# Kernel optimization log

Hardware: AMD Instinct MI355X
Metric: run time of the kernel (lower is better)

## Reference

```python
import jax, jax.numpy as jnp
import numpy as np

B, CH_IN, D, H, W = 8, 256, 64, 16, 16
S = CH_IN // 2  # shurink = 128


def setup_inputs() -> dict:
    key = jax.random.key(0)
    ks = jax.random.split(key, 9)
    kstd = (2.0 / CH_IN) ** 0.5   # kaiming-like for 1x1 conv, fan_in = CH_IN
    ostd = (2.0 / S) ** 0.5
    x = jax.random.normal(ks[0], (B, CH_IN, D, H, W), dtype=jnp.float32)
    wk = jax.random.normal(ks[1], (S, CH_IN), dtype=jnp.float32) * kstd
    wq = jax.random.normal(ks[2], (S, CH_IN), dtype=jnp.float32) * kstd
    wv = jax.random.normal(ks[3], (S, CH_IN), dtype=jnp.float32) * kstd
    wo = jax.random.normal(ks[4], (CH_IN, S), dtype=jnp.float32) * ostd
    bk = jax.random.normal(ks[5], (S,), dtype=jnp.float32) * 0.01
    bq = jax.random.normal(ks[6], (S,), dtype=jnp.float32) * 0.01
    bv = jax.random.normal(ks[7], (S,), dtype=jnp.float32) * 0.01
    bo = jax.random.normal(ks[8], (CH_IN,), dtype=jnp.float32) * 0.01
    return {"x": x, "wk": wk, "bk": bk, "wq": wq, "bq": bq,
            "wv": wv, "bv": bv, "wo": wo, "bo": bo}


def reference(x, wk, bk, wq, bq, wv, bv, wo, bo):
    # 1x1x1 Conv3d == channel contraction: [B,C,D,H,W] x [S,C] -> [B,S,D,H,W]
    def proj(w, b):
        return jnp.einsum('bcdhw,oc->bodhw', x, w) + b[None, :, None, None, None]

    k = proj(wk, bk)  # [B,S,D,H,W]
    q = proj(wq, bq)
    v = proj(wv, bv)
    s_dim = k.shape[1]
    scale = 1.0 / jnp.sqrt(jnp.asarray(s_dim, x.dtype))
    # torch: bmm(k^T, q) over per-(b,h,w) [S,D] matrices -> [D_i, D_j]
    scores = jnp.einsum('bsihw,bsjhw->bhwij', k, q) * scale  # [B,H,W,D,D]
    # torch softmax(dim=1) on [BHW, D, D] == softmax over i (keys axis)
    a = jax.nn.softmax(scores, axis=3)
    # torch: bmm(v, a) -> [S, D_j]
    att = jnp.einsum('bsihw,bhwij->bsjhw', v, a)  # [B,S,D,H,W]
    out = jnp.einsum('bsdhw,cs->bcdhw', att, wo) + bo[None, :, None, None, None]
    return x + out  # atten_factor = 1
```

## Files before the change

### kernel.cpp

```cpp
#include <hip/hip_runtime.h>
#include <hip/hip_bf16.h>


typedef __bf16 bf16_t;
typedef bf16_t bf16x8 __attribute__((ext_vector_type(8)));
typedef bf16_t bf16x4 __attribute__((ext_vector_type(4)));
typedef float  f32x4  __attribute__((ext_vector_type(4)));

#define NB   8
#define NC   256
#define ND   64
#define NHW  256
#define NS   128

#define MFMA16 __builtin_amdgcn_mfma_f32_16x16x32_bf16

__device__ __forceinline__ int swz(int row, int col) {
  return col ^ ((row & 7) << 3);
}

__device__ __forceinline__ bf16x8 pack8(float4 a, float4 b) {
  bf16x8 r;
  r[0] = (bf16_t)a.x; r[1] = (bf16_t)a.y; r[2] = (bf16_t)a.z; r[3] = (bf16_t)a.w;
  r[4] = (bf16_t)b.x; r[5] = (bf16_t)b.y; r[6] = (bf16_t)b.z; r[7] = (bf16_t)b.w;
  return r;
}

__device__ __forceinline__ bf16x8 ldg_w8(const float* p) {
  float4 a = *(const float4*)p;
  float4 b = *(const float4*)(p + 4);
  return pack8(a, b);
}

__global__ __launch_bounds__(256) void transpose_x_w(
    const float* __restrict__ x,
    const float* __restrict__ wk, const float* __restrict__ wq,
    const float* __restrict__ wv, const float* __restrict__ wo,
    bf16_t* __restrict__ xT, bf16_t* __restrict__ wsW) {
  __shared__ bf16_t tile[64 * 72];
  const int bid = blockIdx.x;
  if (bid >= 8192) {
    const int wid = bid - 8192;
    const int mat = wid >> 3, sub = wid & 7;
    const int t = threadIdx.x;
    if (mat < 3) {
      const float* src = (mat == 0) ? wk : (mat == 1) ? wq : wv;
      bf16_t* dst = wsW + mat * 32768;
      int s = sub * 16 + (t >> 4), c0 = (t & 15) * 16;
      const float* p = src + s * NC + c0;
      float4 a0 = *(const float4*)p, a1 = *(const float4*)(p + 4);
      float4 a2 = *(const float4*)(p + 8), a3 = *(const float4*)(p + 12);
      *(bf16x8*)(dst + (c0 >> 3) * 1024 + s * 8)       = pack8(a0, a1);
      *(bf16x8*)(dst + ((c0 >> 3) + 1) * 1024 + s * 8) = pack8(a2, a3);
    } else {
      bf16_t* dst = wsW + 98304;
      int c = sub * 32 + (t >> 3), sc0 = (t & 7) * 16;
      const float* p = wo + c * NS + sc0;
      float4 a0 = *(const float4*)p, a1 = *(const float4*)(p + 4);
      float4 a2 = *(const float4*)(p + 8), a3 = *(const float4*)(p + 12);
      *(bf16x8*)(dst + (sc0 >> 3) * 2048 + c * 8)       = pack8(a0, a1);
      *(bf16x8*)(dst + ((sc0 >> 3) + 1) * 2048 + c * 8) = pack8(a2, a3);
    }
    return;
  }
  const int ct = bid & 3, hwt = (bid >> 2) & 3;
  const int d = (bid >> 4) & 63, b = bid >> 10;
  const int c0 = ct * 64, hw0 = hwt * 64;
  const int t = threadIdx.x;
  const int hwq = t & 15, chi = t >> 4;

  #pragma unroll
  for (int q = 0; q < 4; ++q) {
    int c = q * 16 + chi;
    float4 v4 = *(const float4*)(x + ((size_t)((b * NC + c0 + c) * ND + d)) * NHW + hw0 + hwq * 4);
    tile[(hwq * 4 + 0) * 72 + c] = (bf16_t)v4.x;
    tile[(hwq * 4 + 1) * 72 + c] = (bf16_t)v4.y;
    tile[(hwq * 4 + 2) * 72 + c] = (bf16_t)v4.z;
    tile[(hwq * 4 + 3) * 72 + c] = (bf16_t)v4.w;
  }
  __syncthreads();
  #pragma unroll
  for (int i = 0; i < 2; ++i) {
    int idx = t + 256 * i;
    int hw = idx >> 3, q = idx & 7;
    bf16x8 v8 = *(const bf16x8*)&tile[hw * 72 + q * 8];
    *(bf16x8*)(xT + ((size_t)((b * ND + d) * NHW + hw0 + hw)) * NC + c0 + q * 8) = v8;
  }
}

__global__ __launch_bounds__(256, 2) void qkv_attn2(
    const bf16_t* __restrict__ xT, const bf16_t* __restrict__ wsW,
    const float* __restrict__ bk, const float* __restrict__ bq,
    const float* __restrict__ bv, bf16_t* __restrict__ att) {
  __shared__ struct {
    union {
      bf16_t xTl[ND * NC];
      struct {
        bf16_t aT[ND * ND];
        bf16_t attT[ND * NS];
      } p2;
    } u;
    bf16_t kT[ND * NS];
    bf16_t qT[ND * NS];
    bf16_t vS[NS * ND];
  } sm;
  const int gid = blockIdx.x;
  const int b = gid & 7, hw = gid >> 3;
  const int t = threadIdx.x, w = t >> 6, lane = t & 63;
  const int l16 = lane & 15, q4 = lane >> 4;

  const bf16_t* wkF = wsW;
  const bf16_t* wqF = wsW + 32768;
  const bf16_t* wvF = wsW + 65536;

  #pragma unroll
  for (int jj = 0; jj < 8; ++jj) {
    int id = jj * 256 + t;
    int d = id >> 5, cg = (id & 31) * 8;
    bf16x8 v8 = *(const bf16x8*)(xT + ((size_t)((b * ND + d) * NHW + hw)) * NC + cg);
    *(bf16x8*)&sm.u.xTl[d * NC + swz(d, cg)] = v8;
  }
  __syncthreads();

  {
    const int mat = w >> 1;
    const int sb = (w & 1) * 64;
    const bf16_t* wm = mat ? wqF : wkF;
    const float* bm = mat ? bq : bk;
    bf16_t* dst = mat ? sm.qT : sm.kT;
    f32x4 acc[4][4] = {};
    for (int ks = 0; ks < 8; ++ks) {
      const int kb = ks * 32 + q4 * 8;
      bf16x8 afr[4];
      #pragma unroll
      for (int mt = 0; mt < 4; ++mt) {
        int s = sb + mt * 16 + l16;
        afr[mt] = *(const bf16x8*)(wm + (kb >> 3) * 1024 + s * 8);
      }
      #pragma unroll
      for (int nt = 0; nt < 4; ++nt) {
        int row = nt * 16 + l16;
        bf16x8 bfr = *(const bf16x8*)&sm.u.xTl[row * NC + swz(row, kb)];
        #pragma unroll
        for (int mt = 0; mt < 4; ++mt)
          acc[mt][nt] = MFMA16(afr[mt], bfr, acc[mt][nt], 0, 0, 0);
      }
    }
    #pragma unroll
    for (int mt = 0; mt < 4; ++mt) {
      int s0 = sb + mt * 16 + q4 * 4;
      float4 b4 = *(const float4*)(bm + s0);
      #pragma unroll
      for (int nt = 0; nt < 4; ++nt) {
        int d = nt * 16 + l16;
        bf16x4 pk;
        pk[0] = (bf16_t)(acc[mt][nt][0] + b4.x);
        pk[1] = (bf16_t)(acc[mt][nt][1] + b4.y);
        pk[2] = (bf16_t)(acc[mt][nt][2] + b4.z);
        pk[3] = (bf16_t)(acc[mt][nt][3] + b4.w);
        *(bf16x4*)&dst[d * NS + swz(d, s0)] = pk;
      }
    }
  }

  {
    const int sb = w * 32;
    f32x4 acc[4][2] = {};
    for (int ks = 0; ks < 8; ++ks) {
      const int kb = ks * 32 + q4 * 8;
      bf16x8 afr[4], bfr[2];
      #pragma unroll
      for (int mt = 0; mt < 4; ++mt) {
        int row = mt * 16 + l16;
        afr[mt] = *(const bf16x8*)&sm.u.xTl[row * NC + swz(row, kb)];
      }
      #pragma unroll
      for (int nt = 0; nt < 2; ++nt) {
        int s = sb + nt * 16 + l16;
        bfr[nt] = *(const bf16x8*)(wvF + (kb >> 3) * 1024 + s * 8);
      }
      #pragma unroll
      for (int nt = 0; nt < 2; ++nt)
        #pragma unroll
        for (int mt = 0; mt < 4; ++mt)
          acc[mt][nt] = MFMA16(afr[mt], bfr[nt], acc[mt][nt], 0, 0, 0);
    }
    #pragma unroll
    for (int nt = 0; nt < 2; ++nt) {
      int s = sb + nt * 16 + l16;
      float bvs = bv[s];
      #pragma unroll
      for (int mt = 0; mt < 4; ++mt) {
        int d0 = mt * 16 + q4 * 4;
        bf16x4 pv;
        pv[0] = (bf16_t)(acc[mt][nt][0] + bvs);
        pv[1] = (bf16_t)(acc[mt][nt][1] + bvs);
        pv[2] = (bf16_t)(acc[mt][nt][2] + bvs);
        pv[3] = (bf16_t)(acc[mt][nt][3] + bvs);
        *(bf16x4*)&sm.vS[s * ND + (d0 ^ ((s & 7) << 3))] = pv;
      }
    }
  }
  __syncthreads();

  {
    f32x4 sacc[4] = {};
    for (int ks = 0; ks < 4; ++ks) {
      const int kb = ks * 32 + q4 * 8;
      int jrow = w * 16 + l16;
      bf16x8 bfr = *(const bf16x8*)&sm.qT[jrow * NS + swz(jrow, kb)];
      #pragma unroll
      for (int it = 0; it < 4; ++it) {
        int irow = it * 16 + l16;
        bf16x8 afr = *(const bf16x8*)&sm.kT[irow * NS + swz(irow, kb)];
        sacc[it] = MFMA16(afr, bfr, sacc[it], 0, 0, 0);
      }
    }
    const float scale = 0.088388347648318447f;
    float ps[16];
    float mx = -1e30f;
    #pragma unroll
    for (int it = 0; it < 4; ++it)
      #pragma unroll
      for (int r = 0; r < 4; ++r) {
        float vv = sacc[it][r] * scale;
        ps[it * 4 + r] = vv;
        mx = fmaxf(mx, vv);
      }
    mx = fmaxf(mx, __shfl_xor(mx, 16));
    mx = fmaxf(mx, __shfl_xor(mx, 32));
    float sum = 0.f;
    #pragma unroll
    for (int i = 0; i < 16; ++i) { ps[i] = __expf(ps[i] - mx); sum += ps[i]; }
    sum += __shfl_xor(sum, 16);
    sum += __shfl_xor(sum, 32);
    float inv = 1.f / sum;
    int j = w * 16 + l16;
    #pragma unroll
    for (int it = 0; it < 4; ++it) {
      bf16x4 pk;
      #pragma unroll
      for (int r = 0; r < 4; ++r) pk[r] = (bf16_t)(ps[it * 4 + r] * inv);
      *(bf16x4*)&sm.u.p2.aT[j * ND + ((it * 16 + q4 * 4) ^ ((j & 7) << 3))] = pk;
    }
  }
  __syncthreads();

  {
    const int sb = w * 32;
    f32x4 acc[2][4] = {};
    #pragma unroll
    for (int ki = 0; ki < 2; ++ki) {
      const int kb = ki * 32 + q4 * 8;
      bf16x8 afr[2];
      #pragma unroll
      for (int mt = 0; mt < 2; ++mt) {
        int srow = sb + mt * 16 + l16;
        afr[mt] = *(const bf16x8*)&sm.vS[srow * ND + (kb ^ ((srow & 7) << 3))];
      }
      #pragma unroll
      for (int nt = 0; nt < 4; ++nt) {
        int jrow = nt * 16 + l16;
        bf16x8 bfr = *(const bf16x8*)&sm.u.p2.aT[jrow * ND + (kb ^ ((jrow & 7) << 3))];
        #pragma unroll
        for (int mt = 0; mt < 2; ++mt)
          acc[mt][nt] = MFMA16(afr[mt], bfr, acc[mt][nt], 0, 0, 0);
      }
    }
    #pragma unroll
    for (int nt = 0; nt < 4; ++nt) {
      int j = nt * 16 + l16;
      #pragma unroll
      for (int mt = 0; mt < 2; ++mt) {
        bf16x4 pk;
        #pragma unroll
        for (int r = 0; r < 4; ++r) pk[r] = (bf16_t)acc[mt][nt][r];
        *(bf16x4*)&sm.u.p2.attT[j * NS + swz(j, sb + mt * 16 + q4 * 4)] = pk;
      }
    }
  }
  __syncthreads();

  #pragma unroll
  for (int jj = 0; jj < 4; ++jj) {
    int f = jj * 2048 + t * 8;
    int d = f >> 7, s0 = f & 127;
    bf16x8 v8 = *(const bf16x8*)&sm.u.p2.attT[d * NS + (s0 ^ ((d & 7) << 3))];
    *(bf16x8*)(att + ((size_t)((b * ND + d) * NHW + hw)) * NS + s0) = v8;
  }
}

__global__ __launch_bounds__(256, 2) void out_proj(
    const bf16_t* __restrict__ att_ws,
    const bf16_t* __restrict__ woF, const float* __restrict__ bo,
    const float* __restrict__ x, float* __restrict__ out) {
  __shared__ union {
    bf16_t slab[256 * 128];
    float  stage[64 * 256];
  } sm;
  const int bid = blockIdx.x;
  const int ht = bid & 7, dc = (bid >> 3) & 7, ch = (bid >> 6) & 1, b = bid >> 7;
  const int t = threadIdx.x, w = t >> 6, lane = t & 63;
  const int l16 = lane & 15, g = lane >> 4;
  const int mh = w >> 1, nh = w & 1;

  {
    const int d = t >> 5, hw = t & 31;
    const bf16_t* src = att_ws + ((size_t)((b * ND + dc * 8 + d) * NHW + ht * 32 + hw)) * NS;
    const int row = d * 32 + hw;
    #pragma unroll
    for (int j = 0; j < 16; ++j) {
      bf16x8 v8 = *(const bf16x8*)(src + j * 8);
      *(bf16x8*)&sm.slab[row * NS + ((j ^ (hw & 7)) << 3)] = v8;
    }
  }
  __syncthreads();

  f32x4 acc[4][8] = {};
  #pragma unroll
  for (int kq = 0; kq < 4; ++kq) {
    bf16x8 af[4];
    #pragma unroll
    for (int mt = 0; mt < 4; ++mt) {
      int c = ch * 128 + mh * 64 + mt * 16 + l16;
      af[mt] = *(const bf16x8*)(woF + (kq * 4 + g) * 2048 + c * 8);
    }
    #pragma unroll
    for (int nt = 0; nt < 8; ++nt) {
      int dl = nh * 4 + (nt >> 1);
      int hwl = (nt & 1) * 16 + l16;
      int row = dl * 32 + hwl;
      bf16x8 bfr = *(const bf16x8*)&sm.slab[row * NS + (((kq * 4 + g) ^ (hwl & 7)) << 3)];
      #pragma unroll
      for (int mt = 0; mt < 4; ++mt)
        acc[mt][nt] = MFMA16(af[mt], bfr, acc[mt][nt], 0, 0, 0);
    }
  }

  #pragma unroll
  for (int p = 0; p < 2; ++p) {
    __syncthreads();
    if (mh == p) {
      #pragma unroll
      for (int mt = 0; mt < 4; ++mt) {
        #pragma unroll
        for (int nt = 0; nt < 8; ++nt) {
          int dl = nh * 4 + (nt >> 1);
          int hws = ((nt & 1) * 16 + l16) ^ (g << 3);
          int base = (mt * 16 + g * 4) * 256 + dl * 32 + hws;
          #pragma unroll
          for (int r = 0; r < 4; ++r)
            sm.stage[base + r * 256] = acc[mt][nt][r];
        }
      }
    }
    __syncthreads();
    #pragma unroll
    for (int ii = 0; ii < 16; ++ii) {
      int c6 = ii * 4 + w;
      int c = ch * 128 + p * 64 + c6;
      int dq = (lane >> 3) & 7;
      int hw4 = (lane & 7) * 4;
      float4 v = *(const float4*)&sm.stage[c6 * 256 + dq * 32 + (hw4 ^ ((ii & 3) << 3))];
      size_t gi = ((size_t)(b * NC + c) * ND + dc * 8 + dq) * NHW + ht * 32 + hw4;
      float4 xv = *(const float4*)(x + gi);
      float bias = bo[c];
      float4 o;
      o.x = v.x + bias + xv.x;
      o.y = v.y + bias + xv.y;
      o.z = v.z + bias + xv.z;
      o.w = v.w + bias + xv.w;
      *(float4*)(out + gi) = o;
    }
  }
}

struct SMemF {
  union {
    bf16_t xT[ND * NC];
    struct { bf16_t aT[ND * ND]; bf16_t attT[ND * NS]; } p2;
  } u;
  bf16_t kT[ND * NS];
  bf16_t qT[ND * NS];
  bf16_t vS[NS * ND];
};

__global__ __launch_bounds__(256) void attn_fused(
    const float* __restrict__ x,
    const float* __restrict__ wk, const float* __restrict__ bk,
    const float* __restrict__ wq, const float* __restrict__ bq,
    const float* __restrict__ wv, const float* __restrict__ bv,
    const float* __restrict__ wo, const float* __restrict__ bo,
    float* __restrict__ out) {
  __shared__ SMemF sm;
  const int gid = blockIdx.x;
  const int b = gid & 7;
  const int hw = gid >> 3;
  const int t = threadIdx.x;
  const int w = t >> 6;
  const int lane = t & 63;
  const int l16 = lane & 15;
  const int q4 = lane >> 4;
  const float* xb = x + (size_t)b * NC * ND * NHW + hw;
  {
    const int d = t & 63;
    const int cb = (t >> 6) * 64;
    for (int jj = 0; jj < 8; ++jj) {
      bf16x8 pk;
      #pragma unroll
      for (int e = 0; e < 8; ++e) {
        int c = cb + jj * 8 + e;
        pk[e] = (bf16_t)xb[(size_t)(c * ND + d) * NHW];
      }
      *(bf16x8*)&sm.u.xT[d * NC + swz(d, cb + jj * 8)] = pk;
    }
  }
  __syncthreads();
  {
    const int mat = w >> 1;
    const int sb = (w & 1) * 64;
    const float* wm = mat ? wq : wk;
    const float* bm = mat ? bq : bk;
    bf16_t* dst = mat ? sm.qT : sm.kT;
    f32x4 acc[4][4] = {};
    for (int ks = 0; ks < 8; ++ks) {
      const int kb = ks * 32 + q4 * 8;
      bf16x8 afr[4];
      #pragma unroll
      for (int mt = 0; mt < 4; ++mt) {
        int row = mt * 16 + l16;
        afr[mt] = *(const bf16x8*)&sm.u.xT[row * NC + swz(row, kb)];
      }
      #pragma unroll
      for (int st = 0; st < 4; ++st) {
        int s = sb + st * 16 + l16;
        bf16x8 bfr = ldg_w8(wm + s * NC + kb);
        #pragma unroll
        for (int mt = 0; mt < 4; ++mt)
          acc[mt][st] = MFMA16(afr[mt], bfr, acc[mt][st], 0, 0, 0);
      }
    }
    #pragma unroll
    for (int st = 0; st < 4; ++st) {
      int s = sb + st * 16 + l16;
      float bias = bm[s];
      #pragma unroll
      for (int mt = 0; mt < 4; ++mt) {
        #pragma unroll
        for (int r = 0; r < 4; ++r) {
          int d = mt * 16 + q4 * 4 + r;
          dst[d * NS + swz(d, s)] = (bf16_t)(acc[mt][st][r] + bias);
        }
      }
    }
  }
  {
    const int sb = w * 32;
    f32x4 acc[2][4] = {};
    for (int ks = 0; ks < 8; ++ks) {
      const int kb = ks * 32 + q4 * 8;
      bf16x8 afr[2];
      #pragma unroll
      for (int mt = 0; mt < 2; ++mt)
        afr[mt] = ldg_w8(wv + (sb + mt * 16 + l16) * NC + kb);
      #pragma unroll
      for (int nt = 0; nt < 4; ++nt) {
        int row = nt * 16 + l16;
        bf16x8 bfr = *(const bf16x8*)&sm.u.xT[row * NC + swz(row, kb)];
        #pragma unroll
        for (int mt = 0; mt < 2; ++mt)
          acc[mt][nt] = MFMA16(afr[mt], bfr, acc[mt][nt], 0, 0, 0);
      }
    }
    #pragma unroll
    for (int mt = 0; mt < 2; ++mt) {
      #pragma unroll
      for (int r = 0; r < 4; ++r) {
        int s = sb + mt * 16 + q4 * 4 + r;
        float bias = bv[s];
        #pragma unroll
        for (int nt = 0; nt < 4; ++nt) {
          int d = nt * 16 + l16;
          sm.vS[s * ND + swz(s, d)] = (bf16_t)(acc[mt][nt][r] + bias);
        }
      }
    }
  }
  __syncthreads();
  {
    f32x4 sacc[4] = {};
    for (int ks = 0; ks < 4; ++ks) {
      const int kb = ks * 32 + q4 * 8;
      int jrow = w * 16 + l16;
      bf16x8 bfr = *(const bf16x8*)&sm.qT[jrow * NS + swz(jrow, kb)];
      #pragma unroll
      for (int it = 0; it < 4; ++it) {
        int irow = it * 16 + l16;
        bf16x8 afr = *(const bf16x8*)&sm.kT[irow * NS + swz(irow, kb)];
        sacc[it] = MFMA16(afr, bfr, sacc[it], 0, 0, 0);
      }
    }
    const float scale = 0.088388347648318447f;
    float ps[16];
    float mx = -1e30f;
    #pragma unroll
    for (int it = 0; it < 4; ++it) {
      #pragma unroll
      for (int r = 0; r < 4; ++r) {
        float vv = sacc[it][r] * scale;
        ps[it * 4 + r] = vv;
        mx = fmaxf(mx, vv);
      }
    }
    mx = fmaxf(mx, __shfl_xor(mx, 16));
    mx = fmaxf(mx, __shfl_xor(mx, 32));
    float sum = 0.f;
    #pragma unroll
    for (int i = 0; i < 16; ++i) { ps[i] = __expf(ps[i] - mx); sum += ps[i]; }
    sum += __shfl_xor(sum, 16);
    sum += __shfl_xor(sum, 32);
    float inv = 1.f / sum;
    int j = w * 16 + l16;
    #pragma unroll
    for (int it = 0; it < 4; ++it) {
      bf16x4 pk;
      #pragma unroll
      for (int r = 0; r < 4; ++r) pk[r] = (bf16_t)(ps[it * 4 + r] * inv);
      *(bf16x4*)&sm.u.p2.aT[j * ND + swz(j, it * 16 + q4 * 4)] = pk;
    }
  }
  __syncthreads();
  {
    const int sb = w * 32;
    f32x4 acc[2][4] = {};
    #pragma unroll
    for (int ki = 0; ki < 2; ++ki) {
      const int kb = ki * 32 + q4 * 8;
      bf16x8 afr[2];
      #pragma unroll
      for (int mt = 0; mt < 2; ++mt) {
        int srow = sb + mt * 16 + l16;
        afr[mt] = *(const bf16x8*)&sm.vS[srow * ND + swz(srow, kb)];
      }
      #pragma unroll
      for (int nt = 0; nt < 4; ++nt) {
        int jrow = nt * 16 + l16;
        bf16x8 bfr = *(const bf16x8*)&sm.u.p2.aT[jrow * ND + swz(jrow, kb)];
        #pragma unroll
        for (int mt = 0; mt < 2; ++mt)
          acc[mt][nt] = MFMA16(afr[mt], bfr, acc[mt][nt], 0, 0, 0);
      }
    }
    #pragma unroll
    for (int nt = 0; nt < 4; ++nt) {
      int j = nt * 16 + l16;
      #pragma unroll
      for (int mt = 0; mt < 2; ++mt) {
        bf16x4 pk;
        #pragma unroll
        for (int r = 0; r < 4; ++r) pk[r] = (bf16_t)acc[mt][nt][r];
        *(bf16x4*)&sm.u.p2.attT[j * NS + swz(j, sb + mt * 16 + q4 * 4)] = pk;
      }
    }
  }
  __syncthreads();
  {
    const int cb = w * 64;
    f32x4 acc[4][4] = {};
    for (int ks = 0; ks < 4; ++ks) {
      const int kb = ks * 32 + q4 * 8;
      bf16x8 afr[4];
      #pragma unroll
      for (int mt = 0; mt < 4; ++mt)
        afr[mt] = ldg_w8(wo + (cb + mt * 16 + l16) * NS + kb);
      #pragma unroll
      for (int nt = 0; nt < 4; ++nt) {
        int jrow = nt * 16 + l16;
        bf16x8 bfr = *(const bf16x8*)&sm.u.p2.attT[jrow * NS + swz(jrow, kb)];
        #pragma unroll
        for (int mt = 0; mt < 4; ++mt)
          acc[mt][nt] = MFMA16(afr[mt], bfr, acc[mt][nt], 0, 0, 0);
      }
    }
    #pragma unroll
    for (int mt = 0; mt < 4; ++mt) {
      #pragma unroll
      for (int r = 0; r < 4; ++r) {
        int c = cb + mt * 16 + q4 * 4 + r;
        float bias = bo[c];
        #pragma unroll
        for (int nt = 0; nt < 4; ++nt) {
          int d = nt * 16 + l16;
          size_t gi = (size_t)(((b * NC + c) * ND + d) * NHW + hw);
          out[gi] = acc[mt][nt][r] + bias + x[gi];
        }
      }
    }
  }
}

extern "C" void kernel_launch(void* const* d_in, const int* in_sizes, int n_in,
                              void* d_out, int out_size, void* d_ws, size_t ws_size,
                              hipStream_t stream) {
  const float* x  = (const float*)d_in[0];
  const float* wk = (const float*)d_in[1];
  const float* bk = (const float*)d_in[2];
  const float* wq = (const float*)d_in[3];
  const float* bq = (const float*)d_in[4];
  const float* wv = (const float*)d_in[5];
  const float* bv = (const float*)d_in[6];
  const float* wo = (const float*)d_in[7];
  const float* bo = (const float*)d_in[8];
  float* out = (float*)d_out;

  const size_t need = (size_t)(131072 + 33554432 + 16777216) * 2;
  if (ws_size >= need) {
    bf16_t* wsW = (bf16_t*)d_ws;
    bf16_t* xT  = wsW + 131072;
    bf16_t* att = xT + 33554432;
    transpose_x_w<<<dim3(8224), dim3(256), 0, stream>>>(x, wk, wq, wv, wo, xT, wsW);
    qkv_attn2<<<dim3(2048), dim3(256), 0, stream>>>(xT, wsW, bk, bq, bv, att);
    out_proj<<<dim3(1024), dim3(256), 0, stream>>>(att, wsW + 98304, bo, x, out);
  } else {
    attn_fused<<<dim3(2048), dim3(256), 0, stream>>>(x, wk, bk, wq, bq, wv, bv, wo, bo, out);
  }
}
```

Measured before the change: 139.8 us.

## Shrink qkv_attn LDS by chunking channel loads and fusing K/Q/V GEMM loops

After: 136.5 us. 2.4% less time.

```diff
diff --git a/kernel.cpp b/kernel.cpp
--- a/kernel.cpp
+++ b/kernel.cpp
@@ -88,136 +88,122 @@
   }
 }
 
-__global__ __launch_bounds__(256, 2) void qkv_attn2(
+__global__ __launch_bounds__(256, 3) void qkv_attn3(
     const bf16_t* __restrict__ xT, const bf16_t* __restrict__ wsW,
     const float* __restrict__ bk, const float* __restrict__ bq,
     const float* __restrict__ bv, bf16_t* __restrict__ att) {
-  __shared__ struct {
-    union {
-      bf16_t xTl[ND * NC];
-      struct {
-        bf16_t aT[ND * ND];
-        bf16_t attT[ND * NS];
-      } p2;
-    } u;
-    bf16_t kT[ND * NS];
-    bf16_t qT[ND * NS];
-    bf16_t vS[NS * ND];
-  } sm;
+  __shared__ bf16_t lds[24576];
+  bf16_t* kT   = lds;
+  bf16_t* qT   = lds + 8192;
+  bf16_t* vS   = lds + 16384;
+  bf16_t* xTl  = lds;
+  bf16_t* aT   = lds;
+  bf16_t* attT = lds + 8192;
+
   const int gid = blockIdx.x;
   const int b = gid & 7, hw = gid >> 3;
   const int t = threadIdx.x, w = t >> 6, lane = t & 63;
   const int l16 = lane & 15, q4 = lane >> 4;
 
-  const bf16_t* wkF = wsW;
-  const bf16_t* wqF = wsW + 32768;
+  const int mat = w >> 1;
+  const int sb = (w & 1) * 64;
+  const bf16_t* wm = mat ? (wsW + 32768) : wsW;
   const bf16_t* wvF = wsW + 65536;
+  const float* bm = mat ? bq : bk;
+  bf16_t* dstKQ = mat ? qT : kT;
+  const int sbv = w * 32;
+
+  f32x4 acc[4][4] = {};
+  f32x4 accv[4][2] = {};
+
+  for (int cc = 0; cc < 2; ++cc) {
+    __syncthreads();
+    #pragma unroll
+    for (int jj = 0; jj < 4; ++jj) {
+      int id = jj * 256 + t;
+      int d = id >> 4, cg = (id & 15) * 8;
+      bf16x8 v8 = *(const bf16x8*)(xT + ((size_t)((b * ND + d) * NHW + hw)) * NC + cc * 128 + cg);
+      *(bf16x8*)&xTl[d * 128 + swz(d, cg)] = v8;
+    }
+    __syncthreads();
+    #pragma unroll
+    for (int ks = 0; ks < 4; ++ks) {
+      const int kb = ks * 32 + q4 * 8;
+      const int kgf = ((cc * 128 + kb) >> 3) * 1024;
+      bf16x8 xfr[4], afk[4], bfv[2];
+      #pragma unroll
+      for (int i = 0; i < 4; ++i) {
+        int row = i * 16 + l16;
+        xfr[i] = *(const bf16x8*)&xTl[row * 128 + swz(row, kb)];
+        int s = sb + i * 16 + l16;
+        afk[i] = *(const bf16x8*)(wm + kgf + s * 8);
+      }
+      #pragma unroll
+      for (int i = 0; i < 2; ++i) {
+        int s = sbv + i * 16 + l16;
+        bfv[i] = *(const bf16x8*)(wvF + kgf + s * 8);
+      }
+      #pragma unroll
+      for (int nt = 0; nt < 4; ++nt)
+        #pragma unroll
+        for (int mt = 0; mt < 4; ++mt)
+          acc[mt][nt] = MFMA16(afk[mt], xfr[nt], acc[mt][nt], 0, 0, 0);
+      #pragma unroll
+      for (int nt = 0; nt < 2; ++nt)
+        #pragma unroll
+        for (int mt = 0; mt < 4; ++mt)
+          accv[mt][nt] = MFMA16(xfr[mt], bfv[nt], accv[mt][nt], 0, 0, 0);
+    }
+  }
+  __syncthreads();
 
   #pragma unroll
-  for (int jj = 0; jj < 8; ++jj) {
-    int id = jj * 256 + t;
-    int d = id >> 5, cg = (id & 31) * 8;
-    bf16x8 v8 = *(const bf16x8*)(xT + ((size_t)((b * ND + d) * NHW + hw)) * NC + cg);
-    *(bf16x8*)&sm.u.xTl[d * NC + swz(d, cg)] = v8;
-  }
-  __syncthreads();
-
-  {
-    const int mat = w >> 1;
-    const int sb = (w & 1) * 64;
-    const bf16_t* wm = mat ? wqF : wkF;
-    const float* bm = mat ? bq : bk;
-    bf16_t* dst = mat ? sm.qT : sm.kT;
-    f32x4 acc[4][4] = {};
-    for (int ks = 0; ks < 8; ++ks) {
-      const int kb = ks * 32 + q4 * 8;
-      bf16x8 afr[4];
-      #pragma unroll
-      for (int mt = 0; mt < 4; ++mt) {
-        int s = sb + mt * 16 + l16;
-        afr[mt] = *(const bf16x8*)(wm + (kb >> 3) * 1024 + s * 8);
-      }
-      #pragma unroll
-      for (int nt = 0; nt < 4; ++nt) {
-        int row = nt * 16 + l16;
-        bf16x8 bfr = *(const bf16x8*)&sm.u.xTl[row * NC + swz(row, kb)];
-        #pragma unroll
-        for (int mt = 0; mt < 4; ++mt)
-          acc[mt][nt] = MFMA16(afr[mt], bfr, acc[mt][nt], 0, 0, 0);
-      }
-    }
+  for (int mt = 0; mt < 4; ++mt) {
+    int s0 = sb + mt * 16 + q4 * 4;
+    float4 b4 = *(const float4*)(bm + s0);
+    #pragma unroll
+    for (int nt = 0; nt < 4; ++nt) {
+      int d = nt * 16 + l16;
+      bf16x4 pk;
+      pk[0] = (bf16_t)(acc[mt][nt][0] + b4.x);
+      pk[1] = (bf16_t)(acc[mt][nt][1] + b4.y);
+      pk[2] = (bf16_t)(acc[mt][nt][2] + b4.z);
+      pk[3] = (bf16_t)(acc[mt][nt][3] + b4.w);
+      *(bf16x4*)&dstKQ[d * NS + swz(d, s0)] = pk;
+    }
+  }
+  #pragma unroll
+  for (int nt = 0; nt < 2; ++nt) {
+    int s = sbv + nt * 16 + l16;
+    float bvs = bv[s];
     #pragma unroll
     for (int mt = 0; mt < 4; ++mt) {
-      int s0 = sb + mt * 16 + q4 * 4;
-      float4 b4 = *(const float4*)(bm + s0);
-      #pragma unroll
-      for (int nt = 0; nt < 4; ++nt) {
-        int d = nt * 16 + l16;
-        bf16x4 pk;
-        pk[0] = (bf16_t)(acc[mt][nt][0] + b4.x);
-        pk[1] = (bf16_t)(acc[mt][nt][1] + b4.y);
-        pk[2] = (bf16_t)(acc[mt][nt][2] + b4.z);
-        pk[3] = (bf16_t)(acc[mt][nt][3] + b4.w);
-        *(bf16x4*)&dst[d * NS + swz(d, s0)] = pk;
-      }
-    }
-  }
-
-  {
-    const int sb = w * 32;
-    f32x4 acc[4][2] = {};
-    for (int ks = 0; ks < 8; ++ks) {
-      const int kb = ks * 32 + q4 * 8;
-      bf16x8 afr[4], bfr[2];
-      #pragma unroll
-      for (int mt = 0; mt < 4; ++mt) {
-        int row = mt * 16 + l16;
-        afr[mt] = *(const bf16x8*)&sm.u.xTl[row * NC + swz(row, kb)];
-      }
-      #pragma unroll
-      for (int nt = 0; nt < 2; ++nt) {
-        int s = sb + nt * 16 + l16;
-        bfr[nt] = *(const bf16x8*)(wvF + (kb >> 3) * 1024 + s * 8);
-      }
-      #pragma unroll
-      for (int nt = 0; nt < 2; ++nt)
-        #pragma unroll
-        for (int mt = 0; mt < 4; ++mt)
-          acc[mt][nt] = MFMA16(afr[mt], bfr[nt], acc[mt][nt], 0, 0, 0);
-    }
-    #pragma unroll
-    for (int nt = 0; nt < 2; ++nt) {
-      int s = sb + nt * 16 + l16;
-      float bvs = bv[s];
-      #pragma unroll
-      for (int mt = 0; mt < 4; ++mt) {
-        int d0 = mt * 16 + q4 * 4;
-        bf16x4 pv;
-        pv[0] = (bf16_t)(acc[mt][nt][0] + bvs);
-        pv[1] = (bf16_t)(acc[mt][nt][1] + bvs);
-        pv[2] = (bf16_t)(acc[mt][nt][2] + bvs);
-        pv[3] = (bf16_t)(acc[mt][nt][3] + bvs);
-        *(bf16x4*)&sm.vS[s * ND + (d0 ^ ((s & 7) << 3))] = pv;
-      }
-    }
-  }
-  __syncthreads();
-
+      int d0 = mt * 16 + q4 * 4;
+      bf16x4 pv;
+      pv[0] = (bf16_t)(accv[mt][nt][0] + bvs);
+      pv[1] = (bf16_t)(accv[mt][nt][1] + bvs);
+      pv[2] = (bf16_t)(accv[mt][nt][2] + bvs);
+      pv[3] = (bf16_t)(accv[mt][nt][3] + bvs);
+      *(bf16x4*)&vS[s * ND + (d0 ^ ((s & 7) << 3))] = pv;
+    }
+  }
+  __syncthreads();
+
+  float ps[16];
   {
     f32x4 sacc[4] = {};
     for (int ks = 0; ks < 4; ++ks) {
       const int kb = ks * 32 + q4 * 8;
       int jrow = w * 16 + l16;
-      bf16x8 bfr = *(const bf16x8*)&sm.qT[jrow * NS + swz(jrow, kb)];
+      bf16x8 bfr = *(const bf16x8*)&qT[jrow * NS + swz(jrow, kb)];
       #pragma unroll
       for (int it = 0; it < 4; ++it) {
         int irow = it * 16 + l16;
-        bf16x8 afr = *(const bf16x8*)&sm.kT[irow * NS + swz(irow, kb)];
+        bf16x8 afr = *(const bf16x8*)&kT[irow * NS + swz(irow, kb)];
         sacc[it] = MFMA16(afr, bfr, sacc[it], 0, 0, 0);
       }
     }
     const float scale = 0.088388347648318447f;
-    float ps[16];
     float mx = -1e30f;
     #pragma unroll
     for (int it = 0; it < 4; ++it)
@@ -235,36 +221,42 @@
     sum += __shfl_xor(sum, 16);
     sum += __shfl_xor(sum, 32);
     float inv = 1.f / sum;
+    #pragma unroll
+    for (int i = 0; i < 16; ++i) ps[i] *= inv;
+  }
+  __syncthreads();
+
+  {
     int j = w * 16 + l16;
     #pragma unroll
     for (int it = 0; it < 4; ++it) {
       bf16x4 pk;
       #pragma unroll
-      for (int r = 0; r < 4; ++r) pk[r] = (bf16_t)(ps[it * 4 + r] * inv);
-      *(bf16x4*)&sm.u.p2.aT[j * ND + ((it * 16 + q4 * 4) ^ ((j & 7) << 3))] = pk;
-    }
-  }
-  __syncthreads();
-
-  {
-    const int sb = w * 32;
-    f32x4 acc[2][4] = {};
+      for (int r = 0; r < 4; ++r) pk[r] = (bf16_t)ps[it * 4 + r];
+      *(bf16x4*)&aT[j * ND + ((it * 16 + q4 * 4) ^ ((j & 7) << 3))] = pk;
+    }
+  }
+  __syncthreads();
+
+  {
+    const int sbp = w * 32;
+    f32x4 pacc[2][4] = {};
     #pragma unroll
     for (int ki = 0; ki < 2; ++ki) {
       const int kb = ki * 32 + q4 * 8;
       bf16x8 afr[2];
       #pragma unroll
       for (int mt = 0; mt < 2; ++mt) {
-        int srow = sb + mt * 16 + l16;
-        afr[mt] = *(const bf16x8*)&sm.vS[srow * ND + (kb ^ ((srow & 7) << 3))];
+        int srow = sbp + mt * 16 + l16;
+        afr[mt] = *(const bf16x8*)&vS[srow * ND + (kb ^ ((srow & 7) << 3))];
       }
       #pragma unroll
       for (int nt = 0; nt < 4; ++nt) {
         int jrow = nt * 16 + l16;
-        bf16x8 bfr = *(const bf16x8*)&sm.u.p2.aT[jrow * ND + (kb ^ ((jrow & 7) << 3))];
+        bf16x8 bfr = *(const bf16x8*)&aT[jrow * ND + (kb ^ ((jrow & 7) << 3))];
         #pragma unroll
         for (int mt = 0; mt < 2; ++mt)
-          acc[mt][nt] = MFMA16(afr[mt], bfr, acc[mt][nt], 0, 0, 0);
+          pacc[mt][nt] = MFMA16(afr[mt], bfr, pacc[mt][nt], 0, 0, 0);
       }
     }
     #pragma unroll
@@ -274,8 +266,8 @@
       for (int mt = 0; mt < 2; ++mt) {
         bf16x4 pk;
         #pragma unroll
-        for (int r = 0; r < 4; ++r) pk[r] = (bf16_t)acc[mt][nt][r];
-        *(bf16x4*)&sm.u.p2.attT[j * NS + swz(j, sb + mt * 16 + q4 * 4)] = pk;
+        for (int r = 0; r < 4; ++r) pk[r] = (bf16_t)pacc[mt][nt][r];
+        *(bf16x4*)&attT[j * NS + swz(j, sbp + mt * 16 + q4 * 4)] = pk;
       }
     }
   }
@@ -285,7 +277,7 @@
   for (int jj = 0; jj < 4; ++jj) {
     int f = jj * 2048 + t * 8;
     int d = f >> 7, s0 = f & 127;
-    bf16x8 v8 = *(const bf16x8*)&sm.u.p2.attT[d * NS + (s0 ^ ((d & 7) << 3))];
+    bf16x8 v8 = *(const bf16x8*)&attT[d * NS + (s0 ^ ((d & 7) << 3))];
     *(bf16x8*)(att + ((size_t)((b * ND + d) * NHW + hw)) * NS + s0) = v8;
   }
 }
@@ -619,7 +611,7 @@
     bf16_t* xT  = wsW + 131072;
     bf16_t* att = xT + 33554432;
     transpose_x_w<<<dim3(8224), dim3(256), 0, stream>>>(x, wk, wq, wv, wo, xT, wsW);
-    qkv_attn2<<<dim3(2048), dim3(256), 0, stream>>>(xT, wsW, bk, bq, bv, att);
+    qkv_attn3<<<dim3(2048), dim3(256), 0, stream>>>(xT, wsW, bk, bq, bv, att);
     out_proj<<<dim3(1024), dim3(256), 0, stream>>>(att, wsW + 98304, bo, x, out);
   } else {
     attn_fused<<<dim3(2048), dim3(256), 0, stream>>>(x, wk, bk, wq, bq, wv, bv, wo, bo, out);
```
